# Optimization experiments

Hardware: AMD Instinct MI355X
Metric: run time of the kernel (lower is better)

Reference implementation:

```python
import jax, jax.numpy as jnp
import numpy as np

BS, L, D, H, NL, ITEM_NUM = 128, 64, 512, 8, 2, 100000
NEG_INF = -10000.0


def _ln(x):
    m = jnp.mean(x, axis=-1, keepdims=True)
    v = jnp.var(x, axis=-1, keepdims=True)
    return (x - m) * jax.lax.rsqrt(v + 1e-5)


def _user_encoder(input_embs, log_mask, pos_emb, qkv_w, out_w, ffn_w1, ffn_w2):
    # SASRec-style causal transformer encoder (post-LN blocks)
    B, S, d = input_embs.shape
    dh = d // H
    x = _ln(input_embs + pos_emb[None, :, :])
    pad = (log_mask != 0)                                  # [B,S]
    causal = jnp.tril(jnp.ones((S, S), dtype=bool))
    attn_ok = causal[None, :, :] & pad[:, None, :]         # [B,S,S]
    bias = jnp.where(attn_ok, 0.0, NEG_INF)[:, None, :, :]  # [B,1,S,S]
    for l in range(NL):
        qkv = x @ qkv_w[l]                                 # [B,S,3d]
        q, k, v = jnp.split(qkv, 3, axis=-1)
        q = q.reshape(B, S, H, dh).transpose(0, 2, 1, 3)
        k = k.reshape(B, S, H, dh).transpose(0, 2, 1, 3)
        v = v.reshape(B, S, H, dh).transpose(0, 2, 1, 3)
        scores = jnp.einsum('bhqd,bhkd->bhqk', q, k) / jnp.sqrt(jnp.asarray(dh, x.dtype)) + bias
        attn = jax.nn.softmax(scores, axis=-1)
        o = jnp.einsum('bhqk,bhkd->bhqd', attn, v).transpose(0, 2, 1, 3).reshape(B, S, d)
        x = _ln(x + o @ out_w[l])
        h = jax.nn.gelu(x @ ffn_w1[l])
        x = _ln(x + h @ ffn_w2[l])
    return x


def setup_inputs() -> dict:
    key = jax.random.key(0)
    ks = jax.random.split(key, 9)
    sample_items_id = jax.random.randint(ks[0], (BS, L + 1), 0, ITEM_NUM + 1)
    log_mask = jax.random.randint(ks[1], (BS, L), 0, 2).astype(jnp.float32)
    emb_table = (jax.random.normal(ks[2], (ITEM_NUM + 1, D), jnp.float32) * 0.02).at[0].set(0.0)
    pos_emb = jax.random.normal(ks[3], (L, D), jnp.float32) * 0.02
    qkv_w = jax.random.normal(ks[4], (NL, D, 3 * D), jnp.float32) * (D ** -0.5)
    out_w = jax.random.normal(ks[5], (NL, D, D), jnp.float32) * (D ** -0.5)
    ffn_w1 = jax.random.normal(ks[6], (NL, D, 4 * D), jnp.float32) * (D ** -0.5)
    ffn_w2 = jax.random.normal(ks[7], (NL, 4 * D, D), jnp.float32) * ((4 * D) ** -0.5)
    pop_prob = jax.random.uniform(ks[8], (ITEM_NUM + 1,), jnp.float32, 1e-6, 1.0)
    return dict(sample_items_id=sample_items_id, log_mask=log_mask, emb_table=emb_table,
                pos_emb=pos_emb, qkv_w=qkv_w, out_w=out_w, ffn_w1=ffn_w1, ffn_w2=ffn_w2,
                pop_prob=pop_prob)


def reference(sample_items_id, log_mask, emb_table, pos_emb, qkv_w, out_w, ffn_w1, ffn_w2, pop_prob):
    bs, l = log_mask.shape
    N = bs * (l + 1)
    items_flat = sample_items_id.reshape(-1)                        # [N]
    debias = jnp.log(pop_prob[items_flat])                          # [N]
    score_embs = emb_table[items_flat]                              # [N, D]
    input_embs = score_embs.reshape(bs, l + 1, -1)
    prec = _user_encoder(input_embs[:, :-1, :], log_mask, pos_emb, qkv_w, out_w, ffn_w1, ffn_w2)
    prec = prec.reshape(bs * l, -1)                                 # [bs*L, D]
    logits = prec @ score_embs.T - debias[None, :]                  # [bs*L, N]
    # padding-column mask (concat(log_mask, ones) == 0)
    pad_cols = jnp.concatenate([log_mask, jnp.ones((bs, 1), log_mask.dtype)], axis=1).reshape(-1) == 0
    logits = jnp.where(pad_cols[None, :], NEG_INF, logits)
    logits = logits.reshape(bs, l, N)
    # in-batch dedup mask: column k masked for batch i if item k appears in batch i's items
    id_list = sample_items_id.reshape(bs, l + 1)
    member = (items_flat[None, :, None] == id_list[:, None, :]).any(-1)   # [bs, N]
    target_col = jnp.arange(bs)[:, None] * (l + 1) + jnp.arange(1, l + 1)[None, :]  # [bs, L]
    is_target = jnp.arange(N)[None, None, :] == target_col[:, :, None]    # [bs, L, N]
    dedup = member[:, None, :] & ~is_target
    logits = jnp.where(dedup, NEG_INF, logits).reshape(bs * l, N)
    labels = target_col.reshape(-1)                                 # [bs*L]
    logp = jax.nn.log_softmax(logits, axis=-1)
    nll = -jnp.take_along_axis(logp, labels[:, None], axis=1)[:, 0]
    valid = (log_mask.reshape(-1) != 0).astype(logits.dtype)
    return (nll * valid).sum() / valid.sum()
```

## Files before the change

kernel.cpp:

```cpp
#include <hip/hip_runtime.h>
#include <hip/hip_bf16.h>
#include <cstdint>
#include <cstddef>

#define NEG_INF -10000.0f

constexpr int BSZ  = 128;
constexpr int SEQ  = 64;
constexpr int DIM  = 512;
constexpr int HEADS = 8;
constexpr int NLAYER = 2;
constexpr int NCOL = BSZ * (SEQ + 1);
constexpr int NROW = BSZ * SEQ;
constexpr float CMAX = 40.0f;

typedef __attribute__((ext_vector_type(8))) short bf16x8;
typedef __attribute__((ext_vector_type(4))) float f32x4;

__device__ __forceinline__ void async_copy16(const void* g, void* l) {
    __builtin_amdgcn_global_load_lds(
        (const __attribute__((address_space(1))) void*)g,
        (__attribute__((address_space(3))) void*)l, 16, 0, 0);
}

__device__ __forceinline__ float b2f(uint16_t u) {
    return __builtin_bit_cast(float, (uint32_t)u << 16);
}
__device__ __forceinline__ uint16_t f2b(float f) {
    __hip_bfloat16 h = __float2bfloat16(f);
    return __builtin_bit_cast(uint16_t, h);
}

__device__ __forceinline__ float gelu_f(float v) {
    float u = 0.7978845608028654f * (v + 0.044715f * v * v * v);
    return 0.5f * v * (1.0f + tanhf(u));
}

__device__ __forceinline__ void swizzle_rc(int id, int& ry, int& cx) {
    ry = (id & 7) * 8 + ((id >> 3) & 7);
    cx = id >> 6;
}

__global__ __launch_bounds__(256) void gather_posln_kernel(
    const int* __restrict__ ids, const float* __restrict__ table,
    const float* __restrict__ pop, const float* __restrict__ pos,
    __hip_bfloat16* __restrict__ sebf, float* __restrict__ debias,
    __hip_bfloat16* __restrict__ xb) {
    const int w = threadIdx.x >> 6, lane = threadIdx.x & 63;
    const int k = blockIdx.x * 4 + w;
    const int b = k / 65, s = k - b * 65;
    const int id = ids[k];
    const float* src = table + (size_t)id * DIM + lane * 8;
    float4 u0 = *(const float4*)src;
    float4 u1 = *(const float4*)(src + 4);
    float v[8] = {u0.x, u0.y, u0.z, u0.w, u1.x, u1.y, u1.z, u1.w};
    bf16x8 se;
    #pragma unroll
    for (int j = 0; j < 8; j++) se[j] = (short)f2b(v[j]);
    *(bf16x8*)((uint16_t*)sebf + (size_t)k * DIM + lane * 8) = se;
    if (lane == 0) debias[k] = logf(pop[id]);
    if (s < 64) {
        const float* pp = pos + (size_t)s * DIM + lane * 8;
        float4 p0 = *(const float4*)pp;
        float4 p1 = *(const float4*)(pp + 4);
        float t[8] = {v[0] + p0.x, v[1] + p0.y, v[2] + p0.z, v[3] + p0.w,
                      v[4] + p1.x, v[5] + p1.y, v[6] + p1.z, v[7] + p1.w};
        float sum = 0.f, sq = 0.f;
        #pragma unroll
        for (int j = 0; j < 8; j++) { sum += t[j]; sq += t[j] * t[j]; }
        #pragma unroll
        for (int off = 32; off > 0; off >>= 1) {
            sum += __shfl_xor(sum, off, 64);
            sq  += __shfl_xor(sq,  off, 64);
        }
        const float mean = sum * (1.0f / 512.0f);
        const float var  = sq * (1.0f / 512.0f) - mean * mean;
        const float rs = rsqrtf(var + 1e-5f);
        bf16x8 o;
        #pragma unroll
        for (int j = 0; j < 8; j++) o[j] = (short)f2b((t[j] - mean) * rs);
        *(bf16x8*)((uint16_t*)xb + (size_t)(b * 64 + s) * DIM + lane * 8) = o;
    }
}

__global__ __launch_bounds__(256) void mask_kernel(
    const int* __restrict__ ids, const float* __restrict__ log_mask,
    uint8_t* __restrict__ colmask, uint8_t* __restrict__ padcol) {
    const int bi = blockIdx.x >> 3, seg = blockIdx.x & 7;
    __shared__ int sid[65];
    if (threadIdx.x < 65) sid[threadIdx.x] = ids[bi * 65 + threadIdx.x];
    __syncthreads();
    const int kend = (seg + 1) * (NCOL / 8);
    for (int k = seg * (NCOL / 8) + threadIdx.x; k < kend; k += 256) {
        const int id = ids[k];
        bool mem = false;
        #pragma unroll
        for (int j = 0; j < 65; j++) mem |= (sid[j] == id);
        const int i2 = k / 65, jj = k - i2 * 65;
        const bool pc = (jj < 64) && (log_mask[i2 * 64 + jj] == 0.0f);
        colmask[(size_t)bi * NCOL + k] = (mem || pc) ? 1 : 0;
        if (bi == 0) padcol[k] = pc ? 1 : 0;
    }
}

__global__ __launch_bounds__(256) void transpose_bf16_kernel(
    const float* __restrict__ W, __hip_bfloat16* __restrict__ WT, int K, int N) {
    __shared__ float tile[32][33];
    const size_t loff = (size_t)blockIdx.z * K * N;
    const int nt = blockIdx.x * 32, kt = blockIdx.y * 32;
    const int c = threadIdx.x & 31, r = threadIdx.x >> 5;
    #pragma unroll
    for (int p = 0; p < 4; p++)
        tile[p * 8 + r][c] = W[loff + (size_t)(kt + p * 8 + r) * N + nt + c];
    __syncthreads();
    #pragma unroll
    for (int p = 0; p < 4; p++)
        WT[loff + (size_t)(nt + p * 8 + r) * K + kt + c] = __float2bfloat16(tile[c][p * 8 + r]);
}

__global__ __launch_bounds__(256) void resid_ln_kernel(
    __hip_bfloat16* __restrict__ xb, const __hip_bfloat16* __restrict__ y) {
    const int w = threadIdx.x >> 6, lane = threadIdx.x & 63;
    const int row = blockIdx.x * 4 + w;
    uint16_t* xp = (uint16_t*)xb + (size_t)row * DIM + lane * 8;
    const uint16_t* yp = (const uint16_t*)y + (size_t)row * DIM + lane * 8;
    bf16x8 xv = *(const bf16x8*)xp;
    bf16x8 yv = *(const bf16x8*)yp;
    float t[8];
    float sum = 0.f, sq = 0.f;
    #pragma unroll
    for (int j = 0; j < 8; j++) {
        t[j] = b2f((uint16_t)xv[j]) + b2f((uint16_t)yv[j]);
        sum += t[j]; sq += t[j] * t[j];
    }
    #pragma unroll
    for (int off = 32; off > 0; off >>= 1) {
        sum += __shfl_xor(sum, off, 64);
        sq  += __shfl_xor(sq,  off, 64);
    }
    const float mean = sum * (1.0f / 512.0f);
    const float var  = sq * (1.0f / 512.0f) - mean * mean;
    const float rs = rsqrtf(var + 1e-5f);
    bf16x8 o;
    #pragma unroll
    for (int j = 0; j < 8; j++) o[j] = (short)f2b((t[j] - mean) * rs);
    *(bf16x8*)xp = o;
}

template<int TN, bool GELU>
__global__ __launch_bounds__(256) void gemm_bt_kernel(
    const __hip_bfloat16* __restrict__ A, const __hip_bfloat16* __restrict__ Bt,
    __hip_bfloat16* __restrict__ C, int N, int K) {
    __shared__ uint16_t As[2][128][32];
    __shared__ uint16_t Bs[2][TN][32];
    const int tid = threadIdx.x, w = tid >> 6, lane = tid & 63;
    const int quad = lane >> 4, l15 = lane & 15;
    constexpr int AI = (TN == 128) ? 4 : 2;
    const int wr = (TN == 128) ? (w >> 1) : w;
    const int wc = (TN == 128) ? (w & 1) : 0;
    const int rowbase = wr * (AI * 16);
    int ry, cx;
    swizzle_rc(blockIdx.x, ry, cx);
    const int row0 = ry * 128, col0 = cx * TN;
    const uint16_t* Ag = (const uint16_t*)A;
    const uint16_t* Bg = (const uint16_t*)Bt;
    const int sr = lane >> 2, sc = (lane & 3) * 8;
    f32x4 acc[AI][4];
    #pragma unroll
    for (int i = 0; i < AI; i++)
        #pragma unroll
        for (int j = 0; j < 4; j++) acc[i][j] = {0.f, 0.f, 0.f, 0.f};

    for (int k0 = 0; k0 < K; k0 += 64) {
        #pragma unroll
        for (int h = 0; h < 2; h++) {
            #pragma unroll
            for (int i = 0; i < 2; i++) {
                const int rb = w * 32 + i * 16;
                async_copy16(Ag + (size_t)(row0 + rb + sr) * K + k0 + h * 32 + sc, &As[h][rb][0]);
            }
            if (TN == 128) {
                #pragma unroll
                for (int i = 0; i < 2; i++) {
                    const int rb = w * 32 + i * 16;
                    async_copy16(Bg + (size_t)(col0 + rb + sr) * K + k0 + h * 32 + sc, &Bs[h][rb][0]);
                }
            } else {
                const int rb = w * 16;
                async_copy16(Bg + (size_t)(col0 + rb + sr) * K + k0 + h * 32 + sc, &Bs[h][rb][0]);
            }
        }
        __syncthreads();
        #pragma unroll
        for (int h = 0; h < 2; h++) {
            bf16x8 af[AI], bfr[4];
            #pragma unroll
            for (int i = 0; i < AI; i++)
                af[i] = *(const bf16x8*)&As[h][rowbase + i * 16 + l15][quad * 8];
            #pragma unroll
            for (int j = 0; j < 4; j++)
                bfr[j] = *(const bf16x8*)&Bs[h][wc * 64 + j * 16 + l15][quad * 8];
            #pragma unroll
            for (int i = 0; i < AI; i++)
                #pragma unroll
                for (int j = 0; j < 4; j++)
                    acc[i][j] = __builtin_amdgcn_mfma_f32_16x16x32_bf16(af[i], bfr[j], acc[i][j], 0, 0, 0);
        }
        __syncthreads();
    }
    #pragma unroll
    for (int i = 0; i < AI; i++) {
        #pragma unroll
        for (int r = 0; r < 4; r++) {
            const int row = row0 + rowbase + i * 16 + quad * 4 + r;
            #pragma unroll
            for (int j = 0; j < 4; j++) {
                const int col = col0 + wc * 64 + j * 16 + l15;
                float v = acc[i][j][r];
                if (GELU) v = gelu_f(v);
                C[(size_t)row * N + col] = __float2bfloat16(v);
            }
        }
    }
}

__global__ __launch_bounds__(256) void attn_mfma_kernel(
    const __hip_bfloat16* __restrict__ qkv, const float* __restrict__ log_mask,
    __hip_bfloat16* __restrict__ obuf) {
    constexpr int QS = 72;
    constexpr int VS32 = 36;
    __shared__ uint16_t Qs[64 * QS];
    __shared__ uint16_t Ks_[64 * QS];
    __shared__ uint16_t Ps[64 * QS];
    __shared__ uint32_t Vt32[64 * VS32];
    __shared__ float mask_s[64];
    const int b = blockIdx.x >> 3, h = blockIdx.x & 7;
    const int tid = threadIdx.x, w = tid >> 6, lane = tid & 63;
    const int quad = lane >> 4, l15 = lane & 15;
    const uint16_t* qg = (const uint16_t*)qkv;

    if (tid < 64) mask_s[tid] = log_mask[b * 64 + tid];
    #pragma unroll
    for (int it = 0; it < 2; it++) {
        const int idx = it * 256 + tid;
        const int s = idx >> 3, c = (idx & 7) * 8;
        const size_t gbase = (size_t)(b * 64 + s) * 1536 + h * 64 + c;
        *(bf16x8*)&Qs[s * QS + c]  = *(const bf16x8*)&qg[gbase];
        *(bf16x8*)&Ks_[s * QS + c] = *(const bf16x8*)&qg[gbase + 512];
    }
    {
        const int sp = tid >> 3;
        const int c = (tid & 7) * 8;
        const size_t gbase = (size_t)(b * 64 + sp * 2) * 1536 + 1024 + h * 64 + c;
        bf16x8 v0 = *(const bf16x8*)&qg[gbase];
        bf16x8 v1 = *(const bf16x8*)&qg[gbase + 1536];
        #pragma unroll
        for (int jj = 0; jj < 8; jj++)
            Vt32[(c + jj) * VS32 + sp] =
                (uint32_t)(uint16_t)v0[jj] | ((uint32_t)(uint16_t)v1[jj] << 16);
    }
    __syncthreads();

    f32x4 sacc[4];
    #pragma unroll
    for (int j = 0; j < 4; j++) sacc[j] = {0.f, 0.f, 0.f, 0.f};
    #pragma unroll
    for (int k0 = 0; k0 < 2; k0++) {
        bf16x8 aq = *(const bf16x8*)&Qs[(w * 16 + l15) * QS + k0 * 32 + quad * 8];
        #pragma unroll
        for (int j = 0; j < 4; j++) {
            bf16x8 bk = *(const bf16x8*)&Ks_[(j * 16 + l15) * QS + k0 * 32 + quad * 8];
            sacc[j] = __builtin_amdgcn_mfma_f32_16x16x32_bf16(aq, bk, sacc[j], 0, 0, 0);
        }
    }
    #pragma unroll
    for (int r = 0; r < 4; r++) {
        const int q = w * 16 + quad * 4 + r;
        float vals[4];
        float vmax = -3.0e38f;
        #pragma unroll
        for (int j = 0; j < 4; j++) {
            const int col = j * 16 + l15;
            const bool ok = (col <= q) && (mask_s[col] != 0.0f);
            float v = sacc[j][r] * 0.125f + (ok ? 0.0f : NEG_INF);
            vals[j] = v;
            vmax = fmaxf(vmax, v);
        }
        #pragma unroll
        for (int off = 1; off < 16; off <<= 1) vmax = fmaxf(vmax, __shfl_xor(vmax, off, 64));
        float e[4], s = 0.f;
        #pragma unroll
        for (int j = 0; j < 4; j++) { e[j] = __expf(vals[j] - vmax); s += e[j]; }
        #pragma unroll
        for (int off = 1; off < 16; off <<= 1) s += __shfl_xor(s, off, 64);
        const float inv = 1.0f / s;
        #pragma unroll
        for (int j = 0; j < 4; j++)
            Ps[q * QS + j * 16 + l15] = f2b(e[j] * inv);
    }
    __syncthreads();

    f32x4 oacc[4];
    #pragma unroll
    for (int j = 0; j < 4; j++) oacc[j] = {0.f, 0.f, 0.f, 0.f};
    #pragma unroll
    for (int k0 = 0; k0 < 2; k0++) {
        bf16x8 ap = *(const bf16x8*)&Ps[(w * 16 + l15) * QS + k0 * 32 + quad * 8];
        #pragma unroll
        for (int j = 0; j < 4; j++) {
            bf16x8 bv = *(const bf16x8*)&Vt32[(j * 16 + l15) * VS32 + k0 * 16 + quad * 4];
            oacc[j] = __builtin_amdgcn_mfma_f32_16x16x32_bf16(ap, bv, oacc[j], 0, 0, 0);
        }
    }
    #pragma unroll
    for (int r = 0; r < 4; r++) {
        const int q = w * 16 + quad * 4 + r;
        #pragma unroll
        for (int j = 0; j < 4; j++) {
            const int d = j * 16 + l15;
            obuf[(size_t)(b * 64 + q) * 512 + h * 64 + d] = __float2bfloat16(oacc[j][r]);
        }
    }
}

__global__ __launch_bounds__(256) void logits_kernel(
    const __hip_bfloat16* __restrict__ A, const __hip_bfloat16* __restrict__ Bt,
    const float* __restrict__ debias, const uint8_t* __restrict__ colmask,
    const uint8_t* __restrict__ padcol,
    float* __restrict__ partials, float* __restrict__ label_logit) {
    __shared__ uint16_t As[2][128][32];
    __shared__ uint16_t Bs[2][128][32];
    __shared__ float deb_s[128];
    __shared__ uint8_t cm_s[2][128];
    __shared__ uint8_t pc_s[128];
    const int tid = threadIdx.x, w = tid >> 6, lane = tid & 63;
    const int quad = lane >> 4, l15 = lane & 15;
    const int wr = w >> 1, wc = w & 1;
    int ry, cx;
    swizzle_rc(blockIdx.x, ry, cx);
    const int row0 = ry * 128, col0 = cx * 128;
    const uint16_t* Ag = (const uint16_t*)A;
    const uint16_t* Bg = (const uint16_t*)Bt;
    const int sr = lane >> 2, sc = (lane & 3) * 8;

    if (tid < 128) {
        deb_s[tid] = debias[col0 + tid];
        pc_s[tid]  = padcol[col0 + tid];
        const int bi0 = row0 >> 6;
        cm_s[0][tid] = colmask[(size_t)bi0 * NCOL + col0 + tid];
        cm_s[1][tid] = colmask[(size_t)(bi0 + 1) * NCOL + col0 + tid];
    }

    f32x4 acc[4][4];
    #pragma unroll
    for (int i = 0; i < 4; i++)
        #pragma unroll
        for (int j = 0; j < 4; j++) acc[i][j] = {0.f, 0.f, 0.f, 0.f};

    for (int k0 = 0; k0 < DIM; k0 += 64) {
        #pragma unroll
        for (int h = 0; h < 2; h++) {
            #pragma unroll
            for (int i = 0; i < 2; i++) {
                const int rb = w * 32 + i * 16;
                async_copy16(Ag + (size_t)(row0 + rb + sr) * DIM + k0 + h * 32 + sc, &As[h][rb][0]);
                async_copy16(Bg + (size_t)(col0 + rb + sr) * DIM + k0 + h * 32 + sc, &Bs[h][rb][0]);
            }
        }
        __syncthreads();
        #pragma unroll
        for (int h = 0; h < 2; h++) {
            bf16x8 af[4], bfr[4];
            #pragma unroll
            for (int i = 0; i < 4; i++) {
                af[i]  = *(const bf16x8*)&As[h][wr * 64 + i * 16 + l15][quad * 8];
                bfr[i] = *(const bf16x8*)&Bs[h][wc * 64 + i * 16 + l15][quad * 8];
            }
            #pragma unroll
            for (int i = 0; i < 4; i++)
                #pragma unroll
                for (int j = 0; j < 4; j++)
                    acc[i][j] = __builtin_amdgcn_mfma_f32_16x16x32_bf16(af[i], bfr[j], acc[i][j], 0, 0, 0);
        }
        __syncthreads();
    }

    #pragma unroll
    for (int i = 0; i < 4; i++) {
        #pragma unroll
        for (int r = 0; r < 4; r++) {
            const int lrow = wr * 64 + i * 16 + quad * 4 + r;
            const int row = row0 + lrow;
            const int bi = row >> 6;
            const int label = bi * 65 + (row & 63) + 1;
            float s = 0.f;
            #pragma unroll
            for (int j = 0; j < 4; j++) {
                const int lcol = wc * 64 + j * 16 + l15;
                const int col = col0 + lcol;
                float v = acc[i][j][r] - deb_s[lcol];
                const bool is_lab = (col == label);
                const bool masked = is_lab ? (pc_s[lcol] != 0) : (cm_s[lrow >> 6][lcol] != 0);
                if (masked) v = NEG_INF;
                if (is_lab) label_logit[row] = v;
                s += __expf(v - CMAX);
            }
            #pragma unroll
            for (int off = 1; off < 16; off <<= 1) s += __shfl_xor(s, off, 64);
            if (l15 == 0) {
                const int strip = (col0 >> 6) + wc;
                partials[(size_t)row * 130 + strip] = s;
            }
        }
    }
}

__global__ __launch_bounds__(256) void combine_kernel(
    const float* __restrict__ partials, const float* __restrict__ label_logit,
    const float* __restrict__ log_mask, float* __restrict__ bsums) {
    const int row = blockIdx.x * 256 + threadIdx.x;
    const float* pr = partials + (size_t)row * 130;
    float Ls = 0.f;
    for (int t = 0; t < 130; t++) Ls += pr[t];
    const float lse = CMAX + logf(Ls);
    const float valid = (log_mask[row] != 0.0f) ? 1.0f : 0.0f;
    float a = (lse - label_logit[row]) * valid;
    float c = valid;
    __shared__ float sa[4], sc_[4];
    #pragma unroll
    for (int off = 32; off > 0; off >>= 1) {
        a += __shfl_down(a, off, 64);
        c += __shfl_down(c, off, 64);
    }
    const int lane = threadIdx.x & 63, w = threadIdx.x >> 6;
    if (lane == 0) { sa[w] = a; sc_[w] = c; }
    __syncthreads();
    if (threadIdx.x == 0) {
        bsums[blockIdx.x * 2 + 0] = sa[0] + sa[1] + sa[2] + sa[3];
        bsums[blockIdx.x * 2 + 1] = sc_[0] + sc_[1] + sc_[2] + sc_[3];
    }
}

__global__ __launch_bounds__(64) void finalize_kernel(
    const float* __restrict__ bsums, float* __restrict__ out) {
    const int t = threadIdx.x;
    float a = 0.f, c = 0.f;
    if (t < 32) { a = bsums[2 * t]; c = bsums[2 * t + 1]; }
    #pragma unroll
    for (int off = 32; off > 0; off >>= 1) {
        a += __shfl_down(a, off, 64);
        c += __shfl_down(c, off, 64);
    }
    if (t == 0) out[0] = a / c;
}

extern "C" void kernel_launch(void* const* d_in, const int* in_sizes, int n_in,
                              void* d_out, int out_size, void* d_ws, size_t ws_size,
                              hipStream_t stream) {
    const int*   ids    = (const int*)d_in[0];
    const float* lm     = (const float*)d_in[1];
    const float* emb    = (const float*)d_in[2];
    const float* pos    = (const float*)d_in[3];
    const float* qkv_w  = (const float*)d_in[4];
    const float* out_w  = (const float*)d_in[5];
    const float* ffn1_w = (const float*)d_in[6];
    const float* ffn2_w = (const float*)d_in[7];
    const float* pop    = (const float*)d_in[8];
    float* out = (float*)d_out;

    char* p = (char*)d_ws;
    auto alloc = [&](size_t bytes) {
        char* r = p;
        p += (bytes + 255) & ~(size_t)255;
        return r;
    };
    typedef __hip_bfloat16 bf16;
    bf16*    sebf     = (bf16*)alloc((size_t)NCOL * DIM * 2);
    float*   debias   = (float*)alloc((size_t)NCOL * 4);
    uint8_t* padcol   = (uint8_t*)alloc(NCOL);
    uint8_t* colmask  = (uint8_t*)alloc((size_t)BSZ * NCOL);
    bf16*    xb       = (bf16*)alloc((size_t)NROW * DIM * 2);
    bf16*    big      = (bf16*)alloc((size_t)NROW * 2048 * 2);
    bf16*    tmp1     = (bf16*)alloc((size_t)NROW * DIM * 2);
    bf16*    tmp2     = (bf16*)alloc((size_t)NROW * DIM * 2);
    float*   partials = (float*)alloc((size_t)NROW * 130 * 4);
    float*   lab      = (float*)alloc((size_t)NROW * 4);
    float*   bsums    = (float*)alloc(64 * 4);
    bf16*    qkvT     = (bf16*)alloc((size_t)NLAYER * 1536 * 512 * 2);
    bf16*    outT     = (bf16*)alloc((size_t)NLAYER * 512 * 512 * 2);
    bf16*    f1T      = (bf16*)alloc((size_t)NLAYER * 2048 * 512 * 2);
    bf16*    f2T      = (bf16*)alloc((size_t)NLAYER * 512 * 2048 * 2);

    transpose_bf16_kernel<<<dim3(1536 / 32, 512 / 32, NLAYER), 256, 0, stream>>>(
        qkv_w, qkvT, 512, 1536);
    transpose_bf16_kernel<<<dim3(512 / 32, 512 / 32, NLAYER), 256, 0, stream>>>(
        out_w, outT, 512, 512);
    transpose_bf16_kernel<<<dim3(2048 / 32, 512 / 32, NLAYER), 256, 0, stream>>>(
        ffn1_w, f1T, 512, 2048);
    transpose_bf16_kernel<<<dim3(512 / 32, 2048 / 32, NLAYER), 256, 0, stream>>>(
        ffn2_w, f2T, 2048, 512);

    gather_posln_kernel<<<NCOL / 4, 256, 0, stream>>>(ids, emb, pop, pos, sebf, debias, xb);
    mask_kernel<<<BSZ * 8, 256, 0, stream>>>(ids, lm, colmask, padcol);

    for (int l = 0; l < NLAYER; l++) {
        gemm_bt_kernel<128, false><<<(1536 / 128) * 64, 256, 0, stream>>>(
            xb, qkvT + (size_t)l * 1536 * 512, big, 1536, 512);
        attn_mfma_kernel<<<BSZ * HEADS, 256, 0, stream>>>(big, lm, tmp1);
        gemm_bt_kernel<64, false><<<(512 / 64) * 64, 256, 0, stream>>>(
            tmp1, outT + (size_t)l * 512 * 512, tmp2, 512, 512);
        resid_ln_kernel<<<NROW / 4, 256, 0, stream>>>(xb, tmp2);
        gemm_bt_kernel<128, true><<<(2048 / 128) * 64, 256, 0, stream>>>(
            xb, f1T + (size_t)l * 2048 * 512, big, 2048, 512);
        gemm_bt_kernel<64, false><<<(512 / 64) * 64, 256, 0, stream>>>(
            big, f2T + (size_t)l * 512 * 2048, tmp2, 512, 2048);
        resid_ln_kernel<<<NROW / 4, 256, 0, stream>>>(xb, tmp2);
    }

    logits_kernel<<<65 * 64, 256, 0, stream>>>(
        xb, sebf, debias, colmask, padcol, partials, lab);
    combine_kernel<<<NROW / 256, 256, 0, stream>>>(partials, lab, lm, bsums);
    finalize_kernel<<<1, 64, 0, stream>>>(bsums, out);
}
```

Measured before the change: 651.8 us.

## Add pipelined 256x256 MFMA GEMM for QKV, FFN1 and logits with split label pass

Adds a 512-thread GEMM kernel that computes 256x256 output tiles. It uses XOR-swizzled double-buffered LDS, async global-to-LDS loads interleaved with MFMA phases, explicit waitcnt and barriers, and s_setprio around the MFMA bursts. The kernel replaces the QKV and FFN1 GEMMs and the fused logits/partial-sum kernel. Columns are padded to 8448 and padded columns are masked, so the logits grid tiles evenly. The label logit moves to a separate dot-product kernel and is added back in the combine step. The aim is higher operand reuse and better overlap of loads with math on the large GEMMs. The cost is 128KB of LDS per block, which limits occupancy, plus more hand-scheduled synchronisation.

```diff
diff --git a/kernel.cpp b/kernel.cpp
--- a/kernel.cpp
+++ b/kernel.cpp
@@ -11,7 +11,9 @@
 constexpr int HEADS = 8;
 constexpr int NLAYER = 2;
 constexpr int NCOL = BSZ * (SEQ + 1);
+constexpr int NCOLP = 8448;
 constexpr int NROW = BSZ * SEQ;
+constexpr int NSTRIP = NCOLP / 64;
 constexpr float CMAX = 40.0f;
 
 typedef __attribute__((ext_vector_type(8))) short bf16x8;
@@ -40,6 +42,10 @@
     ry = (id & 7) * 8 + ((id >> 3) & 7);
     cx = id >> 6;
 }
+
+#define BAR() __builtin_amdgcn_s_barrier()
+#define LGKM0() asm volatile("s_waitcnt lgkmcnt(0)" ::: "memory")
+#define VMCNT(n) asm volatile("s_waitcnt vmcnt(" #n ")" ::: "memory")
 
 __global__ __launch_bounds__(256) void gather_posln_kernel(
     const int* __restrict__ ids, const float* __restrict__ table,
@@ -90,16 +96,21 @@
     __shared__ int sid[65];
     if (threadIdx.x < 65) sid[threadIdx.x] = ids[bi * 65 + threadIdx.x];
     __syncthreads();
-    const int kend = (seg + 1) * (NCOL / 8);
-    for (int k = seg * (NCOL / 8) + threadIdx.x; k < kend; k += 256) {
-        const int id = ids[k];
-        bool mem = false;
-        #pragma unroll
-        for (int j = 0; j < 65; j++) mem |= (sid[j] == id);
-        const int i2 = k / 65, jj = k - i2 * 65;
-        const bool pc = (jj < 64) && (log_mask[i2 * 64 + jj] == 0.0f);
-        colmask[(size_t)bi * NCOL + k] = (mem || pc) ? 1 : 0;
-        if (bi == 0) padcol[k] = pc ? 1 : 0;
+    const int kend = (seg + 1) * (NCOLP / 8);
+    for (int k = seg * (NCOLP / 8) + threadIdx.x; k < kend; k += 256) {
+        uint8_t cmv, pcv;
+        if (k < NCOL) {
+            const int id = ids[k];
+            bool mem = false;
+            #pragma unroll
+            for (int j = 0; j < 65; j++) mem |= (sid[j] == id);
+            const int i2 = k / 65, jj = k - i2 * 65;
+            const bool pc = (jj < 64) && (log_mask[i2 * 64 + jj] == 0.0f);
+            cmv = (mem || pc) ? 1 : 0;
+            pcv = pc ? 1 : 0;
+        } else { cmv = 1; pcv = 1; }
+        colmask[(size_t)bi * NCOLP + k] = cmv;
+        if (bi == 0) padcol[k] = pcv;
     }
 }
 
@@ -323,108 +334,286 @@
     }
 }
 
-__global__ __launch_bounds__(256) void logits_kernel(
+template<int EPI>
+__global__ __launch_bounds__(512) void gemm256_kernel(
     const __hip_bfloat16* __restrict__ A, const __hip_bfloat16* __restrict__ Bt,
+    __hip_bfloat16* __restrict__ C, int N, int K,
     const float* __restrict__ debias, const uint8_t* __restrict__ colmask,
-    const uint8_t* __restrict__ padcol,
-    float* __restrict__ partials, float* __restrict__ label_logit) {
-    __shared__ uint16_t As[2][128][32];
-    __shared__ uint16_t Bs[2][128][32];
-    __shared__ float deb_s[128];
-    __shared__ uint8_t cm_s[2][128];
-    __shared__ uint8_t pc_s[128];
-    const int tid = threadIdx.x, w = tid >> 6, lane = tid & 63;
+    float* __restrict__ partials) {
+    __shared__ uint16_t SA[2][2][128 * 64];
+    __shared__ uint16_t SB[2][2][128 * 64];
+    __shared__ float dc_s[256];
+    __shared__ uint8_t cm_s[4][256];
+
+    const int tid = threadIdx.x;
+    const int w = tid >> 6, lane = tid & 63;
     const int quad = lane >> 4, l15 = lane & 15;
-    const int wr = w >> 1, wc = w & 1;
-    int ry, cx;
-    swizzle_rc(blockIdx.x, ry, cx);
-    const int row0 = ry * 128, col0 = cx * 128;
+    const int wr = w >> 2, wc = w & 3;
+
+    const int nwg = gridDim.x;
+    const int xid = (blockIdx.x & 7) * (nwg >> 3) + (blockIdx.x >> 3);
+    const int ry = xid & 31, cx = xid >> 5;
+    const int row0 = ry * 256, col0 = cx * 256;
+
     const uint16_t* Ag = (const uint16_t*)A;
     const uint16_t* Bg = (const uint16_t*)Bt;
-    const int sr = lane >> 2, sc = (lane & 3) * 8;
-
-    if (tid < 128) {
-        deb_s[tid] = debias[col0 + tid];
-        pc_s[tid]  = padcol[col0 + tid];
-        const int bi0 = row0 >> 6;
-        cm_s[0][tid] = colmask[(size_t)bi0 * NCOL + col0 + tid];
-        cm_s[1][tid] = colmask[(size_t)(bi0 + 1) * NCOL + col0 + tid];
-    }
-
-    f32x4 acc[4][4];
-    #pragma unroll
-    for (int i = 0; i < 4; i++)
-        #pragma unroll
-        for (int j = 0; j < 4; j++) acc[i][j] = {0.f, 0.f, 0.f, 0.f};
-
-    for (int k0 = 0; k0 < DIM; k0 += 64) {
+
+    if (EPI == 2) {
+        if (tid < 256) dc_s[tid] = debias[col0 + tid] + CMAX;
+        #pragma unroll
+        for (int j = 0; j < 2; j++) {
+            const int e = j * 512 + tid;
+            cm_s[e >> 8][e & 255] =
+                colmask[(size_t)((row0 >> 6) + (e >> 8)) * NCOLP + col0 + (e & 255)];
+        }
+    }
+
+    const int tb0 = w << 6, tb1 = 512 + (w << 6);
+    const uint16_t* gA[2][2];
+    const uint16_t* gB[2][2];
+    #pragma unroll
+    for (int j = 0; j < 2; j++) {
+        const int t = j * 512 + (w << 6) + lane;
+        const int r = t >> 3;
+        const int s = (t & 7) ^ (r & 7);
         #pragma unroll
         for (int h = 0; h < 2; h++) {
-            #pragma unroll
-            for (int i = 0; i < 2; i++) {
-                const int rb = w * 32 + i * 16;
-                async_copy16(Ag + (size_t)(row0 + rb + sr) * DIM + k0 + h * 32 + sc, &As[h][rb][0]);
-                async_copy16(Bg + (size_t)(col0 + rb + sr) * DIM + k0 + h * 32 + sc, &Bs[h][rb][0]);
-            }
-        }
-        __syncthreads();
-        #pragma unroll
-        for (int h = 0; h < 2; h++) {
-            bf16x8 af[4], bfr[4];
-            #pragma unroll
-            for (int i = 0; i < 4; i++) {
-                af[i]  = *(const bf16x8*)&As[h][wr * 64 + i * 16 + l15][quad * 8];
-                bfr[i] = *(const bf16x8*)&Bs[h][wc * 64 + i * 16 + l15][quad * 8];
-            }
-            #pragma unroll
-            for (int i = 0; i < 4; i++)
+            gA[h][j] = Ag + (size_t)(row0 + h * 128 + r) * K + s * 8;
+            gB[h][j] = Bg + (size_t)(col0 + h * 128 + r) * K + s * 8;
+        }
+    }
+
+    #define STAGE_A(tile, half, k0) do { \
+        async_copy16(gA[half][0] + (k0), &SA[tile][half][tb0 * 8]); \
+        async_copy16(gA[half][1] + (k0), &SA[tile][half][tb1 * 8]); } while (0)
+    #define STAGE_B(tile, half, k0) do { \
+        async_copy16(gB[half][0] + (k0), &SB[tile][half][tb0 * 8]); \
+        async_copy16(gB[half][1] + (k0), &SB[tile][half][tb1 * 8]); } while (0)
+
+    auto fragA = [&](int tile, int m, int kk) -> bf16x8 {
+        return *(const bf16x8*)&SA[tile][wr]
+            [((m * 16 + l15) << 6) + ((((kk << 2) + quad) ^ (l15 & 7)) << 3)];
+    };
+    auto fragB = [&](int tile, int n, int kk) -> bf16x8 {
+        return *(const bf16x8*)&SB[tile][wc >> 1]
+            [(((wc & 1) * 64 + n * 16 + l15) << 6) + ((((kk << 2) + quad) ^ (l15 & 7)) << 3)];
+    };
+
+    f32x4 acc[8][4];
+    #pragma unroll
+    for (int m = 0; m < 8; m++)
+        #pragma unroll
+        for (int n = 0; n < 4; n++) acc[m][n] = {0.f, 0.f, 0.f, 0.f};
+
+    STAGE_A(0, 0, 0); STAGE_A(0, 1, 0);
+    STAGE_B(0, 0, 0); STAGE_B(0, 1, 0);
+    STAGE_A(1, 0, 64); STAGE_B(1, 0, 64);
+    VMCNT(4);
+    BAR();
+
+    const int niters = K >> 7;
+    bf16x8 af[4][2], bA[2][2], bB[2][2];
+    for (int it = 0; it < niters; ++it) {
+        const bool st = (it + 1 < niters);
+        const int kc = it << 7;
+        const int kn = kc + 128;
+
+        #pragma unroll
+        for (int m = 0; m < 4; m++) { af[m][0] = fragA(0, m, 0); af[m][1] = fragA(0, m, 1); }
+        #pragma unroll
+        for (int n = 0; n < 2; n++) { bA[n][0] = fragB(0, n, 0); bA[n][1] = fragB(0, n, 1); }
+        STAGE_A(1, 1, kc + 64);
+        BAR(); LGKM0();
+        __builtin_amdgcn_s_setprio(1);
+        #pragma unroll
+        for (int m = 0; m < 4; m++)
+            #pragma unroll
+            for (int n = 0; n < 2; n++) {
+                acc[m][n] = __builtin_amdgcn_mfma_f32_16x16x32_bf16(af[m][0], bA[n][0], acc[m][n], 0, 0, 0);
+                acc[m][n] = __builtin_amdgcn_mfma_f32_16x16x32_bf16(af[m][1], bA[n][1], acc[m][n], 0, 0, 0);
+            }
+        __builtin_amdgcn_s_setprio(0);
+        BAR();
+
+        #pragma unroll
+        for (int n = 0; n < 2; n++) { bB[n][0] = fragB(0, n + 2, 0); bB[n][1] = fragB(0, n + 2, 1); }
+        STAGE_B(1, 1, kc + 64);
+        BAR(); LGKM0();
+        __builtin_amdgcn_s_setprio(1);
+        #pragma unroll
+        for (int m = 0; m < 4; m++)
+            #pragma unroll
+            for (int n = 0; n < 2; n++) {
+                acc[m][n + 2] = __builtin_amdgcn_mfma_f32_16x16x32_bf16(af[m][0], bB[n][0], acc[m][n + 2], 0, 0, 0);
+                acc[m][n + 2] = __builtin_amdgcn_mfma_f32_16x16x32_bf16(af[m][1], bB[n][1], acc[m][n + 2], 0, 0, 0);
+            }
+        __builtin_amdgcn_s_setprio(0);
+        BAR();
+
+        #pragma unroll
+        for (int m = 0; m < 4; m++) { af[m][0] = fragA(0, m + 4, 0); af[m][1] = fragA(0, m + 4, 1); }
+        if (st) STAGE_B(0, 0, kn);
+        BAR(); LGKM0();
+        __builtin_amdgcn_s_setprio(1);
+        #pragma unroll
+        for (int m = 0; m < 4; m++)
+            #pragma unroll
+            for (int n = 0; n < 2; n++) {
+                acc[m + 4][n + 2] = __builtin_amdgcn_mfma_f32_16x16x32_bf16(af[m][0], bB[n][0], acc[m + 4][n + 2], 0, 0, 0);
+                acc[m + 4][n + 2] = __builtin_amdgcn_mfma_f32_16x16x32_bf16(af[m][1], bB[n][1], acc[m + 4][n + 2], 0, 0, 0);
+            }
+        __builtin_amdgcn_s_setprio(0);
+        BAR();
+
+        if (st) STAGE_A(0, 0, kn);
+        __builtin_amdgcn_s_setprio(1);
+        #pragma unroll
+        for (int m = 0; m < 4; m++)
+            #pragma unroll
+            for (int n = 0; n < 2; n++) {
+                acc[m + 4][n] = __builtin_amdgcn_mfma_f32_16x16x32_bf16(af[m][0], bA[n][0], acc[m + 4][n], 0, 0, 0);
+                acc[m + 4][n] = __builtin_amdgcn_mfma_f32_16x16x32_bf16(af[m][1], bA[n][1], acc[m + 4][n], 0, 0, 0);
+            }
+        __builtin_amdgcn_s_setprio(0);
+        if (st) { VMCNT(4); } else { VMCNT(0); }
+        BAR();
+
+        #pragma unroll
+        for (int m = 0; m < 4; m++) { af[m][0] = fragA(1, m, 0); af[m][1] = fragA(1, m, 1); }
+        #pragma unroll
+        for (int n = 0; n < 2; n++) { bA[n][0] = fragB(1, n, 0); bA[n][1] = fragB(1, n, 1); }
+        if (st) STAGE_A(0, 1, kn);
+        BAR(); LGKM0();
+        __builtin_amdgcn_s_setprio(1);
+        #pragma unroll
+        for (int m = 0; m < 4; m++)
+            #pragma unroll
+            for (int n = 0; n < 2; n++) {
+                acc[m][n] = __builtin_amdgcn_mfma_f32_16x16x32_bf16(af[m][0], bA[n][0], acc[m][n], 0, 0, 0);
+                acc[m][n] = __builtin_amdgcn_mfma_f32_16x16x32_bf16(af[m][1], bA[n][1], acc[m][n], 0, 0, 0);
+            }
+        __builtin_amdgcn_s_setprio(0);
+        BAR();
+
+        #pragma unroll
+        for (int n = 0; n < 2; n++) { bB[n][0] = fragB(1, n + 2, 0); bB[n][1] = fragB(1, n + 2, 1); }
+        if (st) STAGE_B(0, 1, kn);
+        BAR(); LGKM0();
+        __builtin_amdgcn_s_setprio(1);
+        #pragma unroll
+        for (int m = 0; m < 4; m++)
+            #pragma unroll
+            for (int n = 0; n < 2; n++) {
+                acc[m][n + 2] = __builtin_amdgcn_mfma_f32_16x16x32_bf16(af[m][0], bB[n][0], acc[m][n + 2], 0, 0, 0);
+                acc[m][n + 2] = __builtin_amdgcn_mfma_f32_16x16x32_bf16(af[m][1], bB[n][1], acc[m][n + 2], 0, 0, 0);
+            }
+        __builtin_amdgcn_s_setprio(0);
+        BAR();
+
+        #pragma unroll
+        for (int m = 0; m < 4; m++) { af[m][0] = fragA(1, m + 4, 0); af[m][1] = fragA(1, m + 4, 1); }
+        if (st) STAGE_B(1, 0, kn + 64);
+        BAR(); LGKM0();
+        __builtin_amdgcn_s_setprio(1);
+        #pragma unroll
+        for (int m = 0; m < 4; m++)
+            #pragma unroll
+            for (int n = 0; n < 2; n++) {
+                acc[m + 4][n + 2] = __builtin_amdgcn_mfma_f32_16x16x32_bf16(af[m][0], bB[n][0], acc[m + 4][n + 2], 0, 0, 0);
+                acc[m + 4][n + 2] = __builtin_amdgcn_mfma_f32_16x16x32_bf16(af[m][1], bB[n][1], acc[m + 4][n + 2], 0, 0, 0);
+            }
+        __builtin_amdgcn_s_setprio(0);
+        BAR();
+
+        if (st) STAGE_A(1, 0, kn + 64);
+        __builtin_amdgcn_s_setprio(1);
+        #pragma unroll
+        for (int m = 0; m < 4; m++)
+            #pragma unroll
+            for (int n = 0; n < 2; n++) {
+                acc[m + 4][n] = __builtin_amdgcn_mfma_f32_16x16x32_bf16(af[m][0], bA[n][0], acc[m + 4][n], 0, 0, 0);
+                acc[m + 4][n] = __builtin_amdgcn_mfma_f32_16x16x32_bf16(af[m][1], bA[n][1], acc[m + 4][n], 0, 0, 0);
+            }
+        __builtin_amdgcn_s_setprio(0);
+        if (st) { VMCNT(4); BAR(); }
+    }
+
+    if (EPI == 2) {
+        const int strip = cx * 4 + wc;
+        #pragma unroll
+        for (int m = 0; m < 8; m++) {
+            #pragma unroll
+            for (int r = 0; r < 4; r++) {
+                const int lrow = wr * 128 + m * 16 + quad * 4 + r;
+                const int row = row0 + lrow;
+                float s = 0.f;
                 #pragma unroll
-                for (int j = 0; j < 4; j++)
-                    acc[i][j] = __builtin_amdgcn_mfma_f32_16x16x32_bf16(af[i], bfr[j], acc[i][j], 0, 0, 0);
-        }
-        __syncthreads();
-    }
-
-    #pragma unroll
-    for (int i = 0; i < 4; i++) {
-        #pragma unroll
-        for (int r = 0; r < 4; r++) {
-            const int lrow = wr * 64 + i * 16 + quad * 4 + r;
-            const int row = row0 + lrow;
-            const int bi = row >> 6;
-            const int label = bi * 65 + (row & 63) + 1;
-            float s = 0.f;
-            #pragma unroll
-            for (int j = 0; j < 4; j++) {
-                const int lcol = wc * 64 + j * 16 + l15;
-                const int col = col0 + lcol;
-                float v = acc[i][j][r] - deb_s[lcol];
-                const bool is_lab = (col == label);
-                const bool masked = is_lab ? (pc_s[lcol] != 0) : (cm_s[lrow >> 6][lcol] != 0);
-                if (masked) v = NEG_INF;
-                if (is_lab) label_logit[row] = v;
-                s += __expf(v - CMAX);
-            }
-            #pragma unroll
-            for (int off = 1; off < 16; off <<= 1) s += __shfl_xor(s, off, 64);
-            if (l15 == 0) {
-                const int strip = (col0 >> 6) + wc;
-                partials[(size_t)row * 130 + strip] = s;
-            }
-        }
-    }
+                for (int n = 0; n < 4; n++) {
+                    const int lcol = wc * 64 + n * 16 + l15;
+                    float t = acc[m][n][r] - dc_s[lcol];
+                    t = (cm_s[lrow >> 6][lcol] != 0) ? -1.0e30f : t;
+                    s += __expf(t);
+                }
+                #pragma unroll
+                for (int off = 1; off < 16; off <<= 1) s += __shfl_xor(s, off, 64);
+                if (l15 == 0) partials[(size_t)row * NSTRIP + strip] = s;
+            }
+        }
+    } else {
+        #pragma unroll
+        for (int m = 0; m < 8; m++) {
+            #pragma unroll
+            for (int r = 0; r < 4; r++) {
+                const int row = row0 + wr * 128 + m * 16 + quad * 4 + r;
+                #pragma unroll
+                for (int n = 0; n < 4; n++) {
+                    const int col = col0 + wc * 64 + n * 16 + l15;
+                    float v = acc[m][n][r];
+                    if (EPI == 1) v = gelu_f(v);
+                    C[(size_t)row * N + col] = __float2bfloat16(v);
+                }
+            }
+        }
+    }
+    #undef STAGE_A
+    #undef STAGE_B
+}
+
+__global__ __launch_bounds__(256) void label_kernel(
+    const __hip_bfloat16* __restrict__ xb, const __hip_bfloat16* __restrict__ sebf,
+    const float* __restrict__ debias, const uint8_t* __restrict__ padcol,
+    float* __restrict__ lab) {
+    const int w = threadIdx.x >> 6, lane = threadIdx.x & 63;
+    const int row = blockIdx.x * 4 + w;
+    const int b = row >> 6, s0 = row & 63;
+    const int k = b * 65 + s0 + 1;
+    const uint16_t* xp = (const uint16_t*)xb + (size_t)row * DIM + lane * 8;
+    const uint16_t* sp = (const uint16_t*)sebf + (size_t)k * DIM + lane * 8;
+    bf16x8 xv = *(const bf16x8*)xp;
+    bf16x8 sv = *(const bf16x8*)sp;
+    float a = 0.f;
+    #pragma unroll
+    for (int j = 0; j < 8; j++) a += b2f((uint16_t)xv[j]) * b2f((uint16_t)sv[j]);
+    #pragma unroll
+    for (int off = 32; off > 0; off >>= 1) a += __shfl_xor(a, off, 64);
+    if (lane == 0)
+        lab[row] = padcol[k] ? NEG_INF : (a - debias[k]);
 }
 
 __global__ __launch_bounds__(256) void combine_kernel(
     const float* __restrict__ partials, const float* __restrict__ label_logit,
     const float* __restrict__ log_mask, float* __restrict__ bsums) {
     const int row = blockIdx.x * 256 + threadIdx.x;
-    const float* pr = partials + (size_t)row * 130;
-    float Ls = 0.f;
-    for (int t = 0; t < 130; t++) Ls += pr[t];
+    const float lab = label_logit[row];
+    float Ls = __expf(lab - CMAX);
+    const float4* pr = (const float4*)(partials + (size_t)row * NSTRIP);
+    for (int t = 0; t < NSTRIP / 4; t++) {
+        float4 v = pr[t];
+        Ls += v.x + v.y + v.z + v.w;
+    }
     const float lse = CMAX + logf(Ls);
     const float valid = (log_mask[row] != 0.0f) ? 1.0f : 0.0f;
-    float a = (lse - label_logit[row]) * valid;
+    float a = (lse - lab) * valid;
     float c = valid;
     __shared__ float sa[4], sc_[4];
     #pragma unroll
@@ -475,15 +664,15 @@
         return r;
     };
     typedef __hip_bfloat16 bf16;
-    bf16*    sebf     = (bf16*)alloc((size_t)NCOL * DIM * 2);
-    float*   debias   = (float*)alloc((size_t)NCOL * 4);
-    uint8_t* padcol   = (uint8_t*)alloc(NCOL);
-    uint8_t* colmask  = (uint8_t*)alloc((size_t)BSZ * NCOL);
+    bf16*    sebf     = (bf16*)alloc((size_t)NCOLP * DIM * 2);
+    float*   debias   = (float*)alloc((size_t)NCOLP * 4);
+    uint8_t* padcol   = (uint8_t*)alloc(NCOLP);
+    uint8_t* colmask  = (uint8_t*)alloc((size_t)BSZ * NCOLP);
     bf16*    xb       = (bf16*)alloc((size_t)NROW * DIM * 2);
     bf16*    big      = (bf16*)alloc((size_t)NROW * 2048 * 2);
     bf16*    tmp1     = (bf16*)alloc((size_t)NROW * DIM * 2);
     bf16*    tmp2     = (bf16*)alloc((size_t)NROW * DIM * 2);
-    float*   partials = (float*)alloc((size_t)NROW * 130 * 4);
+    float*   partials = (float*)alloc((size_t)NROW * NSTRIP * 4);
     float*   lab      = (float*)alloc((size_t)NROW * 4);
     float*   bsums    = (float*)alloc(64 * 4);
     bf16*    qkvT     = (bf16*)alloc((size_t)NLAYER * 1536 * 512 * 2);
@@ -504,21 +693,22 @@
     mask_kernel<<<BSZ * 8, 256, 0, stream>>>(ids, lm, colmask, padcol);
 
     for (int l = 0; l < NLAYER; l++) {
-        gemm_bt_kernel<128, false><<<(1536 / 128) * 64, 256, 0, stream>>>(
-            xb, qkvT + (size_t)l * 1536 * 512, big, 1536, 512);
+        gemm256_kernel<0><<<32 * (1536 / 256), 512, 0, stream>>>(
+            xb, qkvT + (size_t)l * 1536 * 512, big, 1536, 512, nullptr, nullptr, nullptr);
         attn_mfma_kernel<<<BSZ * HEADS, 256, 0, stream>>>(big, lm, tmp1);
         gemm_bt_kernel<64, false><<<(512 / 64) * 64, 256, 0, stream>>>(
             tmp1, outT + (size_t)l * 512 * 512, tmp2, 512, 512);
         resid_ln_kernel<<<NROW / 4, 256, 0, stream>>>(xb, tmp2);
-        gemm_bt_kernel<128, true><<<(2048 / 128) * 64, 256, 0, stream>>>(
-            xb, f1T + (size_t)l * 2048 * 512, big, 2048, 512);
+        gemm256_kernel<1><<<32 * (2048 / 256), 512, 0, stream>>>(
+            xb, f1T + (size_t)l * 2048 * 512, big, 2048, 512, nullptr, nullptr, nullptr);
         gemm_bt_kernel<64, false><<<(512 / 64) * 64, 256, 0, stream>>>(
             big, f2T + (size_t)l * 512 * 2048, tmp2, 512, 2048);
         resid_ln_kernel<<<NROW / 4, 256, 0, stream>>>(xb, tmp2);
     }
 
-    logits_kernel<<<65 * 64, 256, 0, stream>>>(
-        xb, sebf, debias, colmask, padcol, partials, lab);
+    label_kernel<<<NROW / 4, 256, 0, stream>>>(xb, sebf, debias, padcol, lab);
+    gemm256_kernel<2><<<32 * (NCOLP / 256), 512, 0, stream>>>(
+        xb, sebf, nullptr, NCOLP, 512, debias, colmask, partials);
     combine_kernel<<<NROW / 256, 256, 0, stream>>>(partials, lab, lm, bsums);
     finalize_kernel<<<1, 64, 0, stream>>>(bsums, out);
 }
```

New measurement: 655.9 us. No clear change (+0.6%).
